# Performance work log

Measured on AMD Instinct MI355X. Metric: run time of the kernel, lower is better.

## Reference

```python
import jax, jax.numpy as jnp
import numpy as np

GAMMAK = 1.0 / 256.0  # 1/(2*d) so kernel values don't underflow for unit-gaussian data


def setup_inputs() -> dict:
    key = jax.random.key(0)
    k1, k2, k3, k4, k5 = jax.random.split(key, 5)
    N, d = 8192, 128
    X = jax.random.normal(k1, (N, d), dtype=jnp.float32)
    y = jax.random.normal(k2, (N - 1, d), dtype=jnp.float32)
    y_next = jax.random.normal(k3, (N - 1, d), dtype=jnp.float32)
    # reset_transform initializes R=eye, t=0; perturb slightly for nontrivial math
    R = jnp.eye(d, dtype=jnp.float32) + 0.01 * jax.random.normal(k4, (d, d), dtype=jnp.float32)
    t = 0.01 * jax.random.normal(k5, (d, 1), dtype=jnp.float32)
    return {"X": X, "y": y, "y_next": y_next, "R": R, "t": t}


def reference(X, y, y_next, R, t):
    # _transform_pts: (R @ y.T + t).T == y @ R.T + t.squeeze()
    yt = y @ R.T + t[:, 0]            # (N-1, d)
    Xb = X[:-1]                        # (N-1, d) kernel base points
    # pairwise_sqeuclidean(Xb, yt), clamped at 0
    sq = jnp.clip(
        jnp.sum(Xb * Xb, axis=1)[:, None]
        + jnp.sum(yt * yt, axis=1)[None, :]
        - 2.0 * (Xb @ yt.T),
        0.0, None,
    )                                  # (N-1, N-1)
    G = jnp.exp(-GAMMAK * sq)
    # diag(1/rowsum) @ G  ==  G / rowsum[:, None]  (avoids explicit NxN diagonal)
    y_pred = (G / jnp.sum(G, axis=1, keepdims=True)) @ X[1:]  # (N-1, d)
    return y_pred
```

## Files before the change

### kernel.cpp

```cpp
#include <hip/hip_runtime.h>
#include <hip/hip_bf16.h>


#define LOG2E 1.44269504088896340736f
#define KNEG (-(1.0f/256.0f)*LOG2E)
#define KA2C (2.0f*(1.0f/256.0f)*LOG2E)

typedef __attribute__((ext_vector_type(4)))  float f32x4;
typedef __attribute__((ext_vector_type(16))) float f32x16;
typedef __attribute__((ext_vector_type(8)))  short bf16x8;

__device__ __forceinline__ unsigned short f2bf(float f) {
  unsigned u = __builtin_bit_cast(unsigned, f);
  u = (u + 0x7fffu + ((u >> 16) & 1u)) >> 16;
  return (unsigned short)u;
}
__device__ __forceinline__ unsigned pk2bf(float a, float b) {
  __hip_bfloat162 h = __float22bfloat162_rn(float2{a, b});
  unsigned u;
  __builtin_memcpy(&u, &h, 4);
  return u;
}
__device__ __forceinline__ bf16x8 pack8(float4 p0, float4 p1) {
  uint4 u;
  u.x = pk2bf(p0.x, p0.y); u.y = pk2bf(p0.z, p0.w);
  u.z = pk2bf(p1.x, p1.y); u.w = pk2bf(p1.z, p1.w);
  return __builtin_bit_cast(bf16x8, u);
}
__device__ __forceinline__ float fast_exp2(float x) {
#if __has_builtin(__builtin_amdgcn_exp2f)
  return __builtin_amdgcn_exp2f(x);
#else
  return exp2f(x);
#endif
}
__device__ __forceinline__ void gl2lds16(const void* g, void* l) {
  __builtin_amdgcn_global_load_lds((const __attribute__((address_space(1))) unsigned int*)g,
                                   (__attribute__((address_space(3))) unsigned int*)l, 16, 0, 0);
}
__device__ __forceinline__ f32x16 mfma_32x32x16(bf16x8 a, bf16x8 b, f32x16 c) {
  return __builtin_amdgcn_mfma_f32_32x32x16_bf16(a, b, c, 0, 0, 0);
}
__device__ __forceinline__ void pl32swap(unsigned &a, unsigned &b) {
#if __has_builtin(__builtin_amdgcn_permlane32_swap)
  auto r = __builtin_amdgcn_permlane32_swap((int)a, (int)b, false, false);
  a = (unsigned)r[0];
  b = (unsigned)r[1];
#else
  unsigned pa = (unsigned)__shfl_xor((int)a, 32, 64);
  unsigned pb = (unsigned)__shfl_xor((int)b, 32, 64);
  bool hi = (threadIdx.x & 32) != 0;
  unsigned na = hi ? pb : a;
  unsigned nb = hi ? b  : pa;
  a = na; b = nb;
#endif
}

#define T_STRIDE 34816
#define V_OFF    18432

__global__ __launch_bounds__(64) void k_prep(const float* __restrict__ y,
                                             const float* __restrict__ R,
                                             const float* __restrict__ t,
                                             const float* __restrict__ X,
                                             unsigned short* __restrict__ ctp) {
  __shared__ char slice[8704];
  const int task = blockIdx.x;
  const int ln = threadIdx.x;
  const int l = ln & 31, h = ln >> 5;

  if (task < 256) {
    unsigned short* ytt = (unsigned short*)slice;
    float* ynf = (float*)(slice + 8448);
    const int T = task >> 1, jcw = task & 1;
    const int rw = task * 32;
    bf16x8 af[8];
    {
      int row = rw + l; if (row > 8190) row = 8190;
      const float* yr = y + (size_t)row * 128;
#pragma unroll
      for (int kc = 0; kc < 8; ++kc) {
        float4 p0 = *(const float4*)(yr + kc*16 + 8*h);
        float4 p1 = *(const float4*)(yr + kc*16 + 8*h + 4);
        af[kc] = pack8(p0, p1);
      }
    }
    f32x16 ac[4];
#pragma unroll
    for (int cc=0; cc<4; ++cc)
#pragma unroll
      for (int i=0;i<16;++i) ac[cc][i] = 0.f;
#pragma unroll
    for (int cc=0; cc<4; ++cc) {
      const float* Rr = R + (size_t)(cc*32 + l) * 128;
#pragma unroll
      for (int kc=0; kc<8; ++kc) {
        float4 p0 = *(const float4*)(Rr + kc*16 + 8*h);
        float4 p1 = *(const float4*)(Rr + kc*16 + 8*h + 4);
        ac[cc] = mfma_32x32x16(af[kc], pack8(p0, p1), ac[cc]);
      }
    }
    float tv0 = t[l], tv1 = t[32+l], tv2 = t[64+l], tv3 = t[96+l];
    float v0[16], v1[16], v2[16], v3[16], ssq[16];
#pragma unroll
    for (int r=0;r<16;++r) {
      v0[r]=ac[0][r]+tv0; v1[r]=ac[1][r]+tv1; v2[r]=ac[2][r]+tv2; v3[r]=ac[3][r]+tv3;
      ssq[r] = v0[r]*v0[r] + v1[r]*v1[r] + v2[r]*v2[r] + v3[r]*v3[r];
    }
#pragma unroll
    for (int off=1; off<32; off<<=1)
#pragma unroll
      for (int r=0;r<16;++r) ssq[r] += __shfl_xor(ssq[r], off, 64);
    if (l < 16) {
      int r = l;
      int grow = rw + (r&3) + 8*(r>>2) + 4*h;
      ynf[(r&3) + 8*(r>>2) + 4*h] = (grow >= 8191) ? -1.0e4f : KNEG * ssq[r];
    }
#pragma unroll
    for (int r=0;r<16;++r) {
      int rloc = (r&3) + 8*(r>>2) + 4*h;
      ytt[rloc*132 +   0 + l] = f2bf(KA2C * v0[r]);
      ytt[rloc*132 +  32 + l] = f2bf(KA2C * v1[r]);
      ytt[rloc*132 +  64 + l] = f2bf(KA2C * v2[r]);
      ytt[rloc*132 +  96 + l] = f2bf(KA2C * v3[r]);
    }
    __syncthreads();
    char* base = (char*)ctp + (size_t)T*T_STRIDE;
#pragma unroll
    for (int kc=0;kc<8;++kc) {
      const unsigned short* s = &ytt[l*132 + kc*16 + 8*h];
      uint2 a = *(const uint2*)(s);
      uint2 b = *(const uint2*)(s + 4);
      uint4 o; o.x=a.x; o.y=a.y; o.z=b.x; o.w=b.y;
      *(uint4*)(base + (jcw*9 + kc)*1024 + ln*16) = o;
    }
    {
      float yn = ynf[l];
      unsigned short hi = f2bf(yn);
      float hif = __builtin_bit_cast(float, (unsigned)hi << 16);
      unsigned short lo = f2bf(yn - hif);
      uint4 o; o.x = (h == 0) ? ((unsigned)hi | ((unsigned)lo << 16)) : 0u;
      o.y = 0u; o.z = 0u; o.w = 0u;
      *(uint4*)(base + (jcw*9 + 8)*1024 + ln*16) = o;
    }
  } else {
    unsigned short* xs = (unsigned short*)slice;
    const int tv_ = task - 256;
    const int T2 = tv_ >> 1, half = tv_ & 1;
    const int xr0 = T2*64 + half*32 + 1;
    {
      int rl = ln >> 1, ch2 = ln & 1;
      int row = xr0 + rl; if (row > 8191) row = 8191;
      const float* src = X + (size_t)row*128 + ch2*64;
      unsigned short* dst = xs + rl*136 + ch2*64;
#pragma unroll
      for (int i=0;i<8;++i) {
        float4 p0 = *(const float4*)(src + i*8);
        float4 p1 = *(const float4*)(src + i*8 + 4);
        uint4 w;
        w.x = pk2bf(p0.x, p0.y); w.y = pk2bf(p0.z, p0.w);
        w.z = pk2bf(p1.x, p1.y); w.w = pk2bf(p1.z, p1.w);
        *(uint4*)(dst + i*8) = w;
      }
    }
    __syncthreads();
    char* base = (char*)ctp + (size_t)T2*T_STRIDE + V_OFF;
#pragma unroll
    for (int ch=0; ch<8; ++ch) {
      int jcl = ch >> 2, cc = ch & 3;
      int lr0 = jcl*16 + 8*h;
      int c = cc*32 + l;
      uint4 o;
      o.x = (unsigned)xs[(lr0+0)*136 + c] | ((unsigned)xs[(lr0+1)*136 + c] << 16);
      o.y = (unsigned)xs[(lr0+2)*136 + c] | ((unsigned)xs[(lr0+3)*136 + c] << 16);
      o.z = (unsigned)xs[(lr0+4)*136 + c] | ((unsigned)xs[(lr0+5)*136 + c] << 16);
      o.w = (unsigned)xs[(lr0+6)*136 + c] | ((unsigned)xs[(lr0+7)*136 + c] << 16);
      int jc16 = half*2 + jcl;
      *(uint4*)(base + (jc16*4 + cc)*1024 + ln*16) = o;
    }
  }
}

__global__ __launch_bounds__(256, 3) void k_main(
    const float* __restrict__ X,
    const unsigned short* __restrict__ ctp,
    float* __restrict__ accp,
    float* __restrict__ rsp,
    int js) {
  __shared__ unsigned short stg[T_STRIDE/2];
  const int tid = threadIdx.x;
  const int wv = tid >> 6, ln = tid & 63;
  const int l = ln & 31, h = ln >> 5;
  const int row = blockIdx.x*128 + wv*32 + l;

  bf16x8 qf[9];
  {
    const float* xr = X + (size_t)row * 128;
#pragma unroll
    for (int kc=0;kc<8;++kc) {
      float4 p0 = *(const float4*)(xr + kc*16 + 8*h);
      float4 p1 = *(const float4*)(xr + kc*16 + 8*h + 4);
      qf[kc] = pack8(p0, p1);
    }
    uint4 o; o.x = (h == 0) ? 0x3F803F80u : 0u; o.y = 0u; o.z = 0u; o.w = 0u;
    qf[8] = __builtin_bit_cast(bf16x8, o);
  }
  f32x16 acc[4];
#pragma unroll
  for (int cc=0;cc<4;++cc)
#pragma unroll
    for (int i=0;i<16;++i) acc[cc][i]=0.f;
  float rs = 0.f;
  const int sp = blockIdx.y;
  const int Tbeg = (sp * 128) / js;
  const int Tend = ((sp + 1) * 128) / js;

  auto dosm = [&](const f32x16& sa, unsigned wx[4], unsigned wy[4]) {
#pragma unroll
    for (int rg=0; rg<4; ++rg) {
      float g0 = fast_exp2(sa[rg*4+0]);
      float g1 = fast_exp2(sa[rg*4+1]);
      float g2 = fast_exp2(sa[rg*4+2]);
      float g3 = fast_exp2(sa[rg*4+3]);
      rs += (g0+g1) + (g2+g3);
      wx[rg] = pk2bf(g0, g1);
      wy[rg] = pk2bf(g2, g3);
    }
  };
  auto dopv = [&](int jcb, unsigned wx[4], unsigned wy[4]) {
#pragma unroll
    for (int jj=0; jj<2; ++jj) {
      unsigned ax = wx[2*jj], bx = wx[2*jj+1];
      unsigned ay = wy[2*jj], by = wy[2*jj+1];
      pl32swap(ax, bx);
      pl32swap(ay, by);
      uint4 gv; gv.x = ax; gv.y = ay; gv.z = bx; gv.w = by;
      bf16x8 pb = __builtin_bit_cast(bf16x8, gv);
#pragma unroll
      for (int cc=0;cc<4;++cc) {
        bf16x8 a2 = *(const bf16x8*)((const char*)stg + V_OFF + ((jcb+jj)*4+cc)*1024 + ln*16);
        acc[cc] = mfma_32x32x16(a2, pb, acc[cc]);
      }
    }
  };

  {
    const char* cb = (const char*)ctp + (size_t)Tbeg*T_STRIDE;
#pragma unroll
    for (int i=0;i<9;++i) {
      int c = wv + 4*i;
      if (c < 34) gl2lds16(cb + c*1024 + ln*16, (char*)stg + c*1024);
    }
  }
  __syncthreads();

  for (int T = Tbeg; T < Tend; ++T) {
    const bool pf = (T+1 < Tend);
    const char* nb = (const char*)ctp + (size_t)(T+1)*T_STRIDE;

    f32x16 sa0, sa1;
#pragma unroll
    for (int i=0;i<16;++i) { sa0[i]=0.f; sa1[i]=0.f; }
#pragma unroll
    for (int kc=0;kc<9;++kc) {
      bf16x8 a0 = *(const bf16x8*)((const char*)stg + kc*1024 + ln*16);
      sa0 = mfma_32x32x16(a0, qf[kc], sa0);
    }
#pragma unroll
    for (int kc=0;kc<9;++kc) {
      bf16x8 a1 = *(const bf16x8*)((const char*)stg + (9+kc)*1024 + ln*16);
      sa1 = mfma_32x32x16(a1, qf[kc], sa1);
    }
    unsigned wx0[4], wy0[4], wx1[4], wy1[4];
    dosm(sa0, wx0, wy0);

    __syncthreads();
    if (pf) {
#pragma unroll
      for (int i=0;i<5;++i) {
        int c = wv + 4*i;
        if (c < 18) gl2lds16(nb + c*1024 + ln*16, (char*)stg + c*1024);
      }
    }
    dosm(sa1, wx1, wy1);
    dopv(0, wx0, wy0);
    dopv(2, wx1, wy1);

    __syncthreads();
    if (pf) {
#pragma unroll
      for (int i=0;i<4;++i) {
        int c = 18 + wv + 4*i;
        gl2lds16(nb + c*1024 + ln*16, (char*)stg + c*1024);
      }
    }
  }
  rs += __shfl_xor(rs, 32, 64);
  if (h == 0) rsp[(size_t)sp*8192 + row] = rs;
#pragma unroll
  for (int cc=0;cc<4;++cc)
#pragma unroll
    for (int r=0;r<16;++r) {
      int c = cc*32 + (r&3) + 8*(r>>2) + 4*h;
      accp[((size_t)sp*128 + c)*8192 + row] = acc[cc][r];
    }
}

__global__ __launch_bounds__(256) void k_fin(const float* __restrict__ accp,
                                             const float* __restrict__ rsp,
                                             float* __restrict__ out,
                                             int js) {
  __shared__ float tr[64*36];
  __shared__ float rinv[64];
  const int tid = threadIdx.x;
  const int r0 = blockIdx.x * 64;
  const int c0 = blockIdx.y * 32;
  if (tid < 64) {
    float s = 0.f;
    for (int sp=0; sp<js; ++sp) s += rsp[(size_t)sp*8192 + r0 + tid];
    rinv[tid] = 1.f / s;
  }
  const int rq = tid & 15, cg = tid >> 4;
  float v[2][4];
#pragma unroll
  for (int cc=0;cc<2;++cc)
#pragma unroll
    for (int k=0;k<4;++k) v[cc][k]=0.f;
#pragma unroll 4
  for (int sp=0; sp<js; ++sp) {
    const float* base = accp + ((size_t)sp*128 + c0 + cg*2)*8192 + r0 + rq*4;
    float4 p0 = *(const float4*)(base);
    float4 p1 = *(const float4*)(base + 8192);
    v[0][0]+=p0.x; v[0][1]+=p0.y; v[0][2]+=p0.z; v[0][3]+=p0.w;
    v[1][0]+=p1.x; v[1][1]+=p1.y; v[1][2]+=p1.z; v[1][3]+=p1.w;
  }
  __syncthreads();
#pragma unroll
  for (int cc=0;cc<2;++cc)
#pragma unroll
    for (int k=0;k<4;++k)
      tr[(rq*4+k)*36 + cg*2+cc] = v[cc][k] * rinv[rq*4+k];
  __syncthreads();
  {
    int r = tid >> 2, q = tid & 3;
    int grow = r0 + r;
    if (grow < 8191) {
      float* dst = out + (size_t)grow*128 + c0 + q*8;
      const float* s2 = &tr[r*36 + q*8];
      *(float4*)(dst)     = *(const float4*)(s2);
      *(float4*)(dst + 4) = *(const float4*)(s2 + 4);
    }
  }
}

extern "C" void kernel_launch(void* const* d_in, const int* in_sizes, int n_in,
                              void* d_out, int out_size, void* d_ws, size_t ws_size,
                              hipStream_t stream) {
  const float* X = (const float*)d_in[0];
  const float* y = (const float*)d_in[1];
  const float* R = (const float*)d_in[3];
  const float* t = (const float*)d_in[4];
  float* out = (float*)d_out;
  char* ws = (char*)d_ws;

  unsigned short* ctp = (unsigned short*)ws;
  size_t rspoff = (size_t)128 * T_STRIDE;
  float* rsp  = (float*)(ws + rspoff);
  size_t accoff = rspoff + 512*1024;
  float* accp = (float*)(ws + accoff);

  int js = 12;
  while (js > 1 && accoff + (size_t)js*128*8192*4 > ws_size) js >>= 1;

  k_prep<<<dim3(512), dim3(64), 0, stream>>>(y, R, t, X, ctp);
  k_main<<<dim3(64, js), dim3(256), 0, stream>>>(X, ctp, accp, rsp, js);
  k_fin<<<dim3(128, 4), dim3(256), 0, stream>>>(accp, rsp, out, js);
}
```

Before: 130.2 us.

## Process two 32-row query tiles per wave to reuse each LDS key/value fragment

Each wave now handles 64 query rows (two 32-row sub-tiles) instead of 32. Every LDS-loaded key and value fragment feeds two MFMAs, which halves LDS read traffic per unit of work and halves the number of times the key stream is fetched from global memory. To compensate for fewer row blocks, the grid is 32 x 16 with more j-splits, and launch bounds drop to 2 blocks per CU because of the doubled accumulator registers. The compute schedule and the prefetch split points are reordered to match. The risks are register pressure and lower occupancy, plus a larger partial-sum buffer for k_fin to reduce.

```diff
diff --git a/kernel.cpp b/kernel.cpp
--- a/kernel.cpp
+++ b/kernel.cpp
@@ -181,7 +181,7 @@
   }
 }
 
-__global__ __launch_bounds__(256, 3) void k_main(
+__global__ __launch_bounds__(256, 2) void k_main(
     const float* __restrict__ X,
     const unsigned short* __restrict__ ctp,
     float* __restrict__ accp,
@@ -191,31 +191,36 @@
   const int tid = threadIdx.x;
   const int wv = tid >> 6, ln = tid & 63;
   const int l = ln & 31, h = ln >> 5;
-  const int row = blockIdx.x*128 + wv*32 + l;
-
-  bf16x8 qf[9];
+  const int rowA = blockIdx.x*256 + wv*64 + l;
+  const int rowB = rowA + 32;
+
+  bf16x8 qfA[8], qfB[8], qf8;
   {
-    const float* xr = X + (size_t)row * 128;
+    const float* xa = X + (size_t)rowA * 128;
+    const float* xb = X + (size_t)rowB * 128;
 #pragma unroll
     for (int kc=0;kc<8;++kc) {
-      float4 p0 = *(const float4*)(xr + kc*16 + 8*h);
-      float4 p1 = *(const float4*)(xr + kc*16 + 8*h + 4);
-      qf[kc] = pack8(p0, p1);
+      float4 a0 = *(const float4*)(xa + kc*16 + 8*h);
+      float4 a1 = *(const float4*)(xa + kc*16 + 8*h + 4);
+      qfA[kc] = pack8(a0, a1);
+      float4 b0 = *(const float4*)(xb + kc*16 + 8*h);
+      float4 b1 = *(const float4*)(xb + kc*16 + 8*h + 4);
+      qfB[kc] = pack8(b0, b1);
     }
     uint4 o; o.x = (h == 0) ? 0x3F803F80u : 0u; o.y = 0u; o.z = 0u; o.w = 0u;
-    qf[8] = __builtin_bit_cast(bf16x8, o);
-  }
-  f32x16 acc[4];
+    qf8 = __builtin_bit_cast(bf16x8, o);
+  }
+  f32x16 accA[4], accB[4];
 #pragma unroll
   for (int cc=0;cc<4;++cc)
 #pragma unroll
-    for (int i=0;i<16;++i) acc[cc][i]=0.f;
-  float rs = 0.f;
+    for (int i=0;i<16;++i) { accA[cc][i]=0.f; accB[cc][i]=0.f; }
+  float rsA = 0.f, rsB = 0.f;
   const int sp = blockIdx.y;
   const int Tbeg = (sp * 128) / js;
   const int Tend = ((sp + 1) * 128) / js;
 
-  auto dosm = [&](const f32x16& sa, unsigned wx[4], unsigned wy[4]) {
+  auto dosm = [&](const f32x16& sa, unsigned wx[4], unsigned wy[4], float& rs) {
 #pragma unroll
     for (int rg=0; rg<4; ++rg) {
       float g0 = fast_exp2(sa[rg*4+0]);
@@ -227,19 +232,40 @@
       wy[rg] = pk2bf(g2, g3);
     }
   };
-  auto dopv = [&](int jcb, unsigned wx[4], unsigned wy[4]) {
+  auto doS = [&](int jc, f32x16& sA, f32x16& sB) {
+#pragma unroll
+    for (int i=0;i<16;++i) { sA[i]=0.f; sB[i]=0.f; }
+#pragma unroll
+    for (int kc=0;kc<8;++kc) {
+      bf16x8 a = *(const bf16x8*)((const char*)stg + (jc*9+kc)*1024 + ln*16);
+      sA = mfma_32x32x16(a, qfA[kc], sA);
+      sB = mfma_32x32x16(a, qfB[kc], sB);
+    }
+    bf16x8 a = *(const bf16x8*)((const char*)stg + (jc*9+8)*1024 + ln*16);
+    sA = mfma_32x32x16(a, qf8, sA);
+    sB = mfma_32x32x16(a, qf8, sB);
+  };
+  auto dopv = [&](int jcb, unsigned wxA[4], unsigned wyA[4],
+                           unsigned wxB[4], unsigned wyB[4]) {
 #pragma unroll
     for (int jj=0; jj<2; ++jj) {
-      unsigned ax = wx[2*jj], bx = wx[2*jj+1];
-      unsigned ay = wy[2*jj], by = wy[2*jj+1];
-      pl32swap(ax, bx);
-      pl32swap(ay, by);
-      uint4 gv; gv.x = ax; gv.y = ay; gv.z = bx; gv.w = by;
-      bf16x8 pb = __builtin_bit_cast(bf16x8, gv);
+      unsigned axA = wxA[2*jj], bxA = wxA[2*jj+1];
+      unsigned ayA = wyA[2*jj], byA = wyA[2*jj+1];
+      pl32swap(axA, bxA);
+      pl32swap(ayA, byA);
+      uint4 gvA; gvA.x = axA; gvA.y = ayA; gvA.z = bxA; gvA.w = byA;
+      bf16x8 pbA = __builtin_bit_cast(bf16x8, gvA);
+      unsigned axB = wxB[2*jj], bxB = wxB[2*jj+1];
+      unsigned ayB = wyB[2*jj], byB = wyB[2*jj+1];
+      pl32swap(axB, bxB);
+      pl32swap(ayB, byB);
+      uint4 gvB; gvB.x = axB; gvB.y = ayB; gvB.z = bxB; gvB.w = byB;
+      bf16x8 pbB = __builtin_bit_cast(bf16x8, gvB);
 #pragma unroll
       for (int cc=0;cc<4;++cc) {
         bf16x8 a2 = *(const bf16x8*)((const char*)stg + V_OFF + ((jcb+jj)*4+cc)*1024 + ln*16);
-        acc[cc] = mfma_32x32x16(a2, pb, acc[cc]);
+        accA[cc] = mfma_32x32x16(a2, pbA, accA[cc]);
+        accB[cc] = mfma_32x32x16(a2, pbB, accB[cc]);
       }
     }
   };
@@ -258,51 +284,48 @@
     const bool pf = (T+1 < Tend);
     const char* nb = (const char*)ctp + (size_t)(T+1)*T_STRIDE;
 
-    f32x16 sa0, sa1;
-#pragma unroll
-    for (int i=0;i<16;++i) { sa0[i]=0.f; sa1[i]=0.f; }
-#pragma unroll
-    for (int kc=0;kc<9;++kc) {
-      bf16x8 a0 = *(const bf16x8*)((const char*)stg + kc*1024 + ln*16);
-      sa0 = mfma_32x32x16(a0, qf[kc], sa0);
-    }
-#pragma unroll
-    for (int kc=0;kc<9;++kc) {
-      bf16x8 a1 = *(const bf16x8*)((const char*)stg + (9+kc)*1024 + ln*16);
-      sa1 = mfma_32x32x16(a1, qf[kc], sa1);
-    }
-    unsigned wx0[4], wy0[4], wx1[4], wy1[4];
-    dosm(sa0, wx0, wy0);
+    f32x16 sA, sB;
+    unsigned wxA[4], wyA[4], wxB[4], wyB[4];
+    doS(0, sA, sB);
+    dosm(sA, wxA, wyA, rsA);
+    dosm(sB, wxB, wyB, rsB);
+    dopv(0, wxA, wyA, wxB, wyB);
+    doS(1, sA, sB);
+    dosm(sA, wxA, wyA, rsA);
+    dosm(sB, wxB, wyB, rsB);
 
     __syncthreads();
     if (pf) {
 #pragma unroll
-      for (int i=0;i<5;++i) {
+      for (int i=0;i<7;++i) {
         int c = wv + 4*i;
-        if (c < 18) gl2lds16(nb + c*1024 + ln*16, (char*)stg + c*1024);
-      }
-    }
-    dosm(sa1, wx1, wy1);
-    dopv(0, wx0, wy0);
-    dopv(2, wx1, wy1);
+        if (c < 26) gl2lds16(nb + c*1024 + ln*16, (char*)stg + c*1024);
+      }
+    }
+    dopv(2, wxA, wyA, wxB, wyB);
 
     __syncthreads();
     if (pf) {
 #pragma unroll
-      for (int i=0;i<4;++i) {
-        int c = 18 + wv + 4*i;
+      for (int i=0;i<2;++i) {
+        int c = 26 + wv + 4*i;
         gl2lds16(nb + c*1024 + ln*16, (char*)stg + c*1024);
       }
     }
   }
-  rs += __shfl_xor(rs, 32, 64);
-  if (h == 0) rsp[(size_t)sp*8192 + row] = rs;
+  rsA += __shfl_xor(rsA, 32, 64);
+  rsB += __shfl_xor(rsB, 32, 64);
+  if (h == 0) {
+    rsp[(size_t)sp*8192 + rowA] = rsA;
+    rsp[(size_t)sp*8192 + rowB] = rsB;
+  }
 #pragma unroll
   for (int cc=0;cc<4;++cc)
 #pragma unroll
     for (int r=0;r<16;++r) {
       int c = cc*32 + (r&3) + 8*(r>>2) + 4*h;
-      accp[((size_t)sp*128 + c)*8192 + row] = acc[cc][r];
+      accp[((size_t)sp*128 + c)*8192 + rowA] = accA[cc][r];
+      accp[((size_t)sp*128 + c)*8192 + rowB] = accB[cc][r];
     }
 }
 
@@ -369,10 +392,10 @@
   size_t accoff = rspoff + 512*1024;
   float* accp = (float*)(ws + accoff);
 
-  int js = 12;
+  int js = 16;
   while (js > 1 && accoff + (size_t)js*128*8192*4 > ws_size) js >>= 1;
 
   k_prep<<<dim3(512), dim3(64), 0, stream>>>(y, R, t, X, ctp);
-  k_main<<<dim3(64, js), dim3(256), 0, stream>>>(X, ctp, accp, rsp, js);
+  k_main<<<dim3(32, js), dim3(256), 0, stream>>>(X, ctp, accp, rsp, js);
   k_fin<<<dim3(128, 4), dim3(256), 0, stream>>>(accp, rsp, out, js);
 }
```

New measurement: 217.5 us. 1.67x slower.

## Double-buffer LDS tile staging in main kernel with one barrier per tile

Applied to the files above, without the earlier changes.

Replaces the single LDS staging buffer, which was refilled in two halves between two barriers, with two buffers. The next tile is prefetched into the alternate buffer at the start of each iteration, so there is only one barrier per tile. This doubles LDS use per block, so launch bounds drop to 2 blocks per CU, and the j-split count goes from 12 to 8. The change trades occupancy and grid parallelism for fewer syncs and longer latency hiding, and it also shrinks the partial-sum traffic into the finish kernel.

```diff
diff --git a/kernel.cpp b/kernel.cpp
--- a/kernel.cpp
+++ b/kernel.cpp
@@ -181,13 +181,13 @@
   }
 }
 
-__global__ __launch_bounds__(256, 3) void k_main(
+__global__ __launch_bounds__(256, 2) void k_main(
     const float* __restrict__ X,
     const unsigned short* __restrict__ ctp,
     float* __restrict__ accp,
     float* __restrict__ rsp,
     int js) {
-  __shared__ unsigned short stg[T_STRIDE/2];
+  __shared__ unsigned short stg[2][T_STRIDE/2];
   const int tid = threadIdx.x;
   const int wv = tid >> 6, ln = tid & 63;
   const int l = ln & 31, h = ln >> 5;
@@ -227,7 +227,7 @@
       wy[rg] = pk2bf(g2, g3);
     }
   };
-  auto dopv = [&](int jcb, unsigned wx[4], unsigned wy[4]) {
+  auto dopv = [&](const char* sb, int jcb, unsigned wx[4], unsigned wy[4]) {
 #pragma unroll
     for (int jj=0; jj<2; ++jj) {
       unsigned ax = wx[2*jj], bx = wx[2*jj+1];
@@ -238,7 +238,7 @@
       bf16x8 pb = __builtin_bit_cast(bf16x8, gv);
 #pragma unroll
       for (int cc=0;cc<4;++cc) {
-        bf16x8 a2 = *(const bf16x8*)((const char*)stg + V_OFF + ((jcb+jj)*4+cc)*1024 + ln*16);
+        bf16x8 a2 = *(const bf16x8*)(sb + V_OFF + ((jcb+jj)*4+cc)*1024 + ln*16);
         acc[cc] = mfma_32x32x16(a2, pb, acc[cc]);
       }
     }
@@ -254,46 +254,40 @@
   }
   __syncthreads();
 
+  int cur = 0;
   for (int T = Tbeg; T < Tend; ++T) {
-    const bool pf = (T+1 < Tend);
-    const char* nb = (const char*)ctp + (size_t)(T+1)*T_STRIDE;
+    const char* sb = (const char*)stg + cur*T_STRIDE;
+    if (T+1 < Tend) {
+      const char* nb = (const char*)ctp + (size_t)(T+1)*T_STRIDE;
+      char* sn = (char*)stg + (cur^1)*T_STRIDE;
+#pragma unroll
+      for (int i=0;i<9;++i) {
+        int c = wv + 4*i;
+        if (c < 34) gl2lds16(nb + c*1024 + ln*16, sn + c*1024);
+      }
+    }
 
     f32x16 sa0, sa1;
 #pragma unroll
     for (int i=0;i<16;++i) { sa0[i]=0.f; sa1[i]=0.f; }
 #pragma unroll
     for (int kc=0;kc<9;++kc) {
-      bf16x8 a0 = *(const bf16x8*)((const char*)stg + kc*1024 + ln*16);
+      bf16x8 a0 = *(const bf16x8*)(sb + kc*1024 + ln*16);
       sa0 = mfma_32x32x16(a0, qf[kc], sa0);
     }
 #pragma unroll
     for (int kc=0;kc<9;++kc) {
-      bf16x8 a1 = *(const bf16x8*)((const char*)stg + (9+kc)*1024 + ln*16);
+      bf16x8 a1 = *(const bf16x8*)(sb + (9+kc)*1024 + ln*16);
       sa1 = mfma_32x32x16(a1, qf[kc], sa1);
     }
     unsigned wx0[4], wy0[4], wx1[4], wy1[4];
     dosm(sa0, wx0, wy0);
+    dosm(sa1, wx1, wy1);
+    dopv(sb, 0, wx0, wy0);
+    dopv(sb, 2, wx1, wy1);
 
     __syncthreads();
-    if (pf) {
-#pragma unroll
-      for (int i=0;i<5;++i) {
-        int c = wv + 4*i;
-        if (c < 18) gl2lds16(nb + c*1024 + ln*16, (char*)stg + c*1024);
-      }
-    }
-    dosm(sa1, wx1, wy1);
-    dopv(0, wx0, wy0);
-    dopv(2, wx1, wy1);
-
-    __syncthreads();
-    if (pf) {
-#pragma unroll
-      for (int i=0;i<4;++i) {
-        int c = 18 + wv + 4*i;
-        gl2lds16(nb + c*1024 + ln*16, (char*)stg + c*1024);
-      }
-    }
+    cur ^= 1;
   }
   rs += __shfl_xor(rs, 32, 64);
   if (h == 0) rsp[(size_t)sp*8192 + row] = rs;
@@ -369,7 +363,7 @@
   size_t accoff = rspoff + 512*1024;
   float* accp = (float*)(ws + accoff);
 
-  int js = 12;
+  int js = 8;
   while (js > 1 && accoff + (size_t)js*128*8192*4 > ws_size) js >>= 1;
 
   k_prep<<<dim3(512), dim3(64), 0, stream>>>(y, R, t, X, ctp);
```

Measured after the change: 130.6 us. Within noise of the previous version (+0.3%).
